# Performance work log

Hardware: AMD Instinct MI355X
Metric: run time of the kernel (lower is better)

## Reference

```python
import jax, jax.numpy as jnp
import numpy as np

N_NODES = 122880  # 4096 graphs * 30 nodes
N_EDGES = 983040


def gcn_conv(x, W, b, src, dst, n):
    """PyG GCNConv: symmetric-normalized aggregation with self-loops."""
    h = x @ W  # [n, out]
    loop = jnp.arange(n, dtype=src.dtype)
    s = jnp.concatenate([src, loop])
    d = jnp.concatenate([dst, loop])
    deg = jnp.zeros((n,), dtype=h.dtype).at[d].add(1.0)  # >=1 due to self loops
    dinv = jax.lax.rsqrt(deg)
    norm = dinv[s] * dinv[d]  # [E+n]
    out = jax.ops.segment_sum(h[s] * norm[:, None], d, num_segments=n)
    return out + b


def setup_inputs() -> dict:
    key = jax.random.key(0)
    ks = jax.random.split(key, 8)
    x = jax.random.normal(ks[0], (N_NODES, 64), dtype=jnp.float32)
    edge_index = jax.random.randint(ks[1], (2, N_EDGES), 0, N_NODES, dtype=jnp.int64)
    W1 = jax.random.normal(ks[2], (64, 128), dtype=jnp.float32) * (1.0 / np.sqrt(64))
    b1 = jnp.zeros((128,), dtype=jnp.float32)
    W2 = jax.random.normal(ks[3], (128, 64), dtype=jnp.float32) * (1.0 / np.sqrt(128))
    b2 = jnp.zeros((64,), dtype=jnp.float32)
    Wfc = jax.random.normal(ks[4], (1920, 1728), dtype=jnp.float32) * (1.0 / np.sqrt(1920))
    bfc = jnp.zeros((1728,), dtype=jnp.float32)
    return {"x": x, "edge_index": edge_index, "W1": W1, "b1": b1,
            "W2": W2, "b2": b2, "Wfc": Wfc, "bfc": bfc}


def reference(x, edge_index, W1, b1, W2, b2, Wfc, bfc):
    n = x.shape[0]
    src, dst = edge_index[0], edge_index[1]
    h = gcn_conv(x, W1, b1, src, dst, n)
    h = jax.nn.relu(h)  # dropout is identity in eval mode
    h = gcn_conv(h, W2, b2, src, dst, n)
    h = jax.nn.relu(h)
    h = h.reshape(-1, 64 * 30)  # [B, 1920], 30 nodes per graph
    return h @ Wfc + bfc  # [B, 1728]
```

## Files before the change

kernel.cpp:

```cpp
#include <hip/hip_runtime.h>
#include <hip/hip_bf16.h>

#define N_NODES 122880
#define N_EDGES 983040
#define NBKT 480
#define BCAP 2560
#define EPB 4096

typedef __hip_bfloat16 bf16;
typedef __attribute__((ext_vector_type(8))) short short8;
typedef __attribute__((ext_vector_type(4))) float floatx4;

__device__ __forceinline__ void gl_lds16(const void* g, void* l) {
    __builtin_amdgcn_global_load_lds(
        (const __attribute__((address_space(1))) void*)g,
        (__attribute__((address_space(3))) void*)l, 16, 0, 0);
}

__device__ __forceinline__ float bflo(unsigned u) {
    return __uint_as_float(u << 16);
}
__device__ __forceinline__ float bfhi(unsigned u) {
    return __uint_as_float(u & 0xffff0000u);
}

__global__ __launch_bounds__(256) void k_psort(const int* __restrict__ ei,
                                               int* __restrict__ gcur,
                                               unsigned* __restrict__ gbuf) {
    __shared__ int cur[NBKT];
    __shared__ int gb[NBKT];
    const int t = threadIdx.x;
    for (int i = t; i < NBKT; i += 256) cur[i] = 0;
    __syncthreads();
    const int base = blockIdx.x * EPB;
    unsigned pay[16];
    short bk[16], pib[16];
#pragma unroll
    for (int j = 0; j < 16; ++j) {
        int e = base + j * 256 + t;
        int d = ei[N_EDGES + e];
        int s = ei[e];
        bk[j] = (short)(d >> 8);
        pay[j] = (unsigned)(d & 255) | ((unsigned)s << 8);
        pib[j] = (short)atomicAdd(&cur[d >> 8], 1);
    }
    __syncthreads();
    for (int i = t; i < NBKT; i += 256) {
        int c = cur[i];
        gb[i] = c ? atomicAdd(&gcur[i * 16], c) : 0;
    }
    __syncthreads();
#pragma unroll
    for (int j = 0; j < 16; ++j) {
        int pos = gb[bk[j]] + pib[j];
        if (pos < BCAP) gbuf[bk[j] * BCAP + pos] = pay[j];
    }
}

__global__ __launch_bounds__(256) void k_bcsr(const int* __restrict__ gcur,
                                              const unsigned* __restrict__ gbuf,
                                              int* __restrict__ adj,
                                              unsigned* __restrict__ co,
                                              float* __restrict__ dinv) {
    __shared__ int hist[256];
    __shared__ int arr[256];
    __shared__ int exc[256];
    const int b = blockIdx.x, t = threadIdx.x;
    hist[t] = 0;
    __syncthreads();
    int E = gcur[b * 16];
    if (E > BCAP) E = BCAP;
    int dl[10], sv[10];
    short pb[10];
    int n = 0;
    for (int idx = t; idx < E; idx += 256) {
        unsigned p = gbuf[b * BCAP + idx];
        dl[n] = p & 255;
        sv[n] = (int)(p >> 8);
        pb[n] = (short)atomicAdd(&hist[dl[n]], 1);
        ++n;
    }
    __syncthreads();
    const int cnt_t = hist[t];
    arr[t] = cnt_t;
    __syncthreads();
    for (int d = 1; d < 256; d <<= 1) {
        int v = (t >= d) ? arr[t - d] : 0;
        __syncthreads();
        arr[t] += v;
        __syncthreads();
    }
    const int ex = arr[t] - cnt_t;
    exc[t] = ex;
    const int node = b * 256 + t;
    co[node] = ((unsigned)ex << 16) | (unsigned)cnt_t;
    dinv[node] = rsqrtf((float)cnt_t + 1.0f);
    __syncthreads();
    for (int j = 0; j < n; ++j)
        adj[b * BCAP + exc[dl[j]] + pb[j]] = sv[j];
}

__global__ __launch_bounds__(256) void k_xtobf(const float* __restrict__ x,
                                               bf16* __restrict__ xb) {
    int t = blockIdx.x * 256 + threadIdx.x;
    const float4 v = ((const float4*)x)[t];
    bf16* o = xb + t * 4;
    o[0] = __float2bfloat16(v.x);
    o[1] = __float2bfloat16(v.y);
    o[2] = __float2bfloat16(v.z);
    o[3] = __float2bfloat16(v.w);
}

__global__ __launch_bounds__(256) void k_convw(const float* __restrict__ W1,
                                               const float* __restrict__ W2,
                                               bf16* __restrict__ W1T,
                                               bf16* __restrict__ W2T) {
    int t = blockIdx.x * 256 + threadIdx.x;
    if (t < 64 * 128) {
        int k = t >> 7, n = t & 127;
        W1T[n * 64 + k] = __float2bfloat16(W1[t]);
    } else {
        int u = t - 64 * 128;
        int k = u >> 6, n = u & 63;
        W2T[n * 128 + k] = __float2bfloat16(W2[u]);
    }
}

__global__ __launch_bounds__(256) void k_transWfc(const float* __restrict__ W,
                                                  bf16* __restrict__ WT) {
    __shared__ float t[32][33];
    int tx = threadIdx.x, ty = threadIdx.y;
    int n0 = blockIdx.x * 32, k0 = blockIdx.y * 32;
#pragma unroll
    for (int j = 0; j < 4; ++j)
        t[ty + j * 8][tx] = W[(long)(k0 + ty + j * 8) * 1728 + n0 + tx];
    __syncthreads();
#pragma unroll
    for (int j = 0; j < 4; ++j)
        WT[(long)(n0 + ty + j * 8) * 1920 + k0 + tx] =
            __float2bfloat16(t[tx][ty + j * 8]);
}

template <bool BIAS_RELU>
__global__ __launch_bounds__(256) void k_agg(const bf16* __restrict__ xb,
                                             const float* __restrict__ dinv,
                                             const unsigned* __restrict__ co,
                                             const int* __restrict__ adj,
                                             const float* __restrict__ bias,
                                             bf16* __restrict__ out) {
    const int wave = threadIdx.x >> 6, lane = threadIdx.x & 63;
    const int half = lane >> 5, l32 = lane & 31;
    const int node = blockIdx.x * 8 + wave * 2 + half;

    const float di = dinv[node];
    const unsigned c_ = co[node];
    int c = (int)(c_ & 0xffffu);
    if (c > 32) c = 32;
    const int* al = adj + (node >> 8) * BCAP + (c_ >> 16);
    int   sl = (l32 < c) ? al[l32]  : 0;
    float wl = (l32 < c) ? dinv[sl] : 0.0f;

    const unsigned us = *(const unsigned*)(xb + ((long)node << 6) + (l32 << 1));
    float acc0 = di * bflo(us);
    float acc1 = di * bfhi(us);

    for (int p0 = 0; p0 < c; p0 += 8) {
        unsigned uu[8];
        float w8[8];
#pragma unroll
        for (int j = 0; j < 8; ++j) {
            int p = p0 + j;
            bool ok = p < c;
            int s = ok ? __shfl(sl, p, 32) : 0;
            w8[j] = ok ? __shfl(wl, p, 32) : 0.0f;
            uu[j] = *(const unsigned*)(xb + ((long)s << 6) + (l32 << 1));
        }
#pragma unroll
        for (int j = 0; j < 8; ++j) {
            acc0 += w8[j] * bflo(uu[j]);
            acc1 += w8[j] * bfhi(uu[j]);
        }
    }

    float r0 = di * acc0, r1 = di * acc1;
    if (BIAS_RELU) {
        r0 = fmaxf(r0 + bias[l32 * 2], 0.0f);
        r1 = fmaxf(r1 + bias[l32 * 2 + 1], 0.0f);
    }
    bf16* o = out + ((long)node << 6) + (l32 << 1);
    o[0] = __float2bfloat16(r0);
    o[1] = __float2bfloat16(r1);
}

template <bool RELU, bool BIAS, typename OutT>
__global__ __launch_bounds__(256) void gemm_bt(const bf16* __restrict__ A,
                                               const bf16* __restrict__ BT,
                                               const float* __restrict__ bias,
                                               OutT* __restrict__ C,
                                               int M, int N, int K) {
    __shared__ __align__(16) bf16 As[128 * 32];
    __shared__ __align__(16) bf16 Bs[64 * 32];
    const int tid = threadIdx.x;
    const int wave = tid >> 6, lane = tid & 63;
    const int quad = lane >> 4, l16 = lane & 15;
    const int bm = blockIdx.x * 128, bn = blockIdx.y * 64;
    const int wm = (wave & 1) * 64, wn = (wave >> 1) * 32;

    floatx4 acc[4][2];
#pragma unroll
    for (int i = 0; i < 4; ++i)
#pragma unroll
        for (int j = 0; j < 2; ++j)
            acc[i][j] = (floatx4){0.f, 0.f, 0.f, 0.f};

    const int r4 = tid >> 2;
    const int ch = (((tid & 3) ^ ((tid >> 3) & 3)) * 8);
    const bf16* gA0 = A + (long)(bm + r4) * K + ch;
    const bf16* gA1 = A + (long)(bm + r4 + 64) * K + ch;
    const bf16* gB  = BT + (long)(bn + r4) * K + ch;
    bf16* lA0 = As + wave * 512;
    bf16* lA1 = As + 2048 + wave * 512;
    bf16* lB  = Bs + wave * 512;

    const int rsw = (l16 >> 1) & 3;

    for (int k0 = 0; k0 < K; k0 += 32) {
        gl_lds16(gA0 + k0, lA0);
        gl_lds16(gA1 + k0, lA1);
        gl_lds16(gB + k0, lB);
        __syncthreads();
        short8 af[4], bfr[2];
#pragma unroll
        for (int im = 0; im < 4; ++im)
            af[im] = *(const short8*)(As + (wm + im * 16 + l16) * 32 +
                                      (quad ^ rsw) * 8);
#pragma unroll
        for (int in = 0; in < 2; ++in)
            bfr[in] = *(const short8*)(Bs + (wn + in * 16 + l16) * 32 +
                                       (quad ^ rsw) * 8);
#pragma unroll
        for (int im = 0; im < 4; ++im)
#pragma unroll
            for (int in = 0; in < 2; ++in)
                acc[im][in] = __builtin_amdgcn_mfma_f32_16x16x32_bf16(
                    af[im], bfr[in], acc[im][in], 0, 0, 0);
        __syncthreads();
    }

#pragma unroll
    for (int in = 0; in < 2; ++in) {
        int gcol = bn + wn + in * 16 + l16;
        float bv = BIAS ? bias[gcol] : 0.0f;
#pragma unroll
        for (int im = 0; im < 4; ++im) {
            int mrow = bm + wm + im * 16 + quad * 4;
#pragma unroll
            for (int r = 0; r < 4; ++r) {
                float v = acc[im][in][r] + bv;
                if (RELU) v = fmaxf(v, 0.0f);
                if constexpr (sizeof(OutT) == 2)
                    C[(long)(mrow + r) * N + gcol] = __float2bfloat16(v);
                else
                    C[(long)(mrow + r) * N + gcol] = v;
            }
        }
    }
}

extern "C" void kernel_launch(void* const* d_in, const int* in_sizes, int n_in,
                              void* d_out, int out_size, void* d_ws, size_t ws_size,
                              hipStream_t stream) {
    const float* x   = (const float*)d_in[0];
    const int*   ei  = (const int*)d_in[1];
    const float* W1  = (const float*)d_in[2];
    const float* b1  = (const float*)d_in[3];
    const float* W2  = (const float*)d_in[4];
    const float* b2  = (const float*)d_in[5];
    const float* Wfc = (const float*)d_in[6];
    const float* bfc = (const float*)d_in[7];

    char* p = (char*)d_ws;
    int*      gcur = (int*)p;      p += (size_t)NBKT * 16 * 4;
    unsigned* gbuf = (unsigned*)p; p += (size_t)NBKT * BCAP * 4;
    int*      adj  = (int*)p;      p += (size_t)NBKT * BCAP * 4;
    unsigned* co   = (unsigned*)p; p += (size_t)N_NODES * 4;
    float*    dinv = (float*)p;    p += (size_t)N_NODES * 4;
    bf16*     xb   = (bf16*)p;     p += (size_t)N_NODES * 64 * 2;
    bf16*     xa   = (bf16*)p;     p += (size_t)N_NODES * 64 * 2;
    bf16*     h1   = (bf16*)p;     p += (size_t)N_NODES * 128 * 2;
    bf16*     W1T  = (bf16*)p;     p += 128 * 64 * 2;
    bf16*     W2T  = (bf16*)p;     p += 64 * 128 * 2;
    bf16*     WfcT = (bf16*)p;     p += (size_t)1728 * 1920 * 2;

    hipMemsetAsync(gcur, 0, (size_t)NBKT * 16 * 4, stream);
    k_psort<<<N_EDGES / EPB, 256, 0, stream>>>(ei, gcur, gbuf);
    k_bcsr<<<NBKT, 256, 0, stream>>>(gcur, gbuf, adj, co, dinv);
    k_xtobf<<<N_NODES * 64 / 4 / 256, 256, 0, stream>>>(x, xb);
    k_convw<<<64, 256, 0, stream>>>(W1, W2, W1T, W2T);
    k_transWfc<<<dim3(54, 60), dim3(32, 8), 0, stream>>>(Wfc, WfcT);

    k_agg<false><<<N_NODES / 8, 256, 0, stream>>>(xb, dinv, co, adj, nullptr, xa);
    gemm_bt<true, true, bf16><<<dim3(960, 2), 256, 0, stream>>>(
        xa, W1T, b1, h1, N_NODES, 128, 64);
    bf16* g = xa;
    gemm_bt<false, false, bf16><<<dim3(960, 1), 256, 0, stream>>>(
        h1, W2T, nullptr, g, N_NODES, 64, 128);
    bf16* h2 = h1;
    k_agg<true><<<N_NODES / 8, 256, 0, stream>>>(g, dinv, co, adj, b2, h2);
    gemm_bt<false, true, float><<<dim3(32, 27), 256, 0, stream>>>(
        h2, WfcT, bfc, (float*)d_out, 4096, 1728, 1920);
}
```

Before: 264.2 us.

## Fuse the two GCN weight GEMMs into one kernel and register-prefetch gemm_bt

Adds a k_mlp kernel that computes relu(xa·W1+b1) for a 128-row tile, keeps the 128-wide intermediate in LDS, and multiplies it by W2 right away. This removes the global write and re-read of the N×128 h1 buffer and one kernel launch. The final FC gemm_bt also changes from direct global-to-LDS loads to loading the next K-slice into registers and then storing it to LDS, so the global load overlaps the MFMAs. The fused kernel uses more LDS (about 51 KB per block), which can lower occupancy.

```diff
diff --git a/kernel.cpp b/kernel.cpp
--- a/kernel.cpp
+++ b/kernel.cpp
@@ -190,6 +190,106 @@
     bf16* o = out + ((long)node << 6) + (l32 << 1);
     o[0] = __float2bfloat16(r0);
     o[1] = __float2bfloat16(r1);
+}
+
+__global__ __launch_bounds__(256) void k_mlp(const bf16* __restrict__ xa,
+                                             const bf16* __restrict__ W1T,
+                                             const bf16* __restrict__ W2T,
+                                             const float* __restrict__ b1,
+                                             bf16* __restrict__ g) {
+    __shared__ __align__(16) bf16 As[128 * 64];
+    __shared__ __align__(16) bf16 C1s[128 * 136];
+    const int tid = threadIdx.x;
+    const int wave = tid >> 6, lane = tid & 63;
+    const int quad = lane >> 4, l16 = lane & 15;
+    const int bm = blockIdx.x * 128;
+    const int wm = (wave & 1) * 64;
+    const int wn1 = (wave >> 1) * 64;
+    const int wn2 = (wave >> 1) * 32;
+
+#pragma unroll
+    for (int q = 0; q < 4; ++q) {
+        int G = q * 256 + tid;
+        int gc = (G & ~7) | ((G & 7) ^ ((G >> 3) & 7));
+        gl_lds16(xa + (long)bm * 64 + gc * 8, As + ((q * 4 + wave) * 64) * 8);
+    }
+    short8 w1f[2][4];
+#pragma unroll
+    for (int kc = 0; kc < 2; ++kc)
+#pragma unroll
+        for (int in = 0; in < 4; ++in)
+            w1f[kc][in] = *(const short8*)(W1T + (wn1 + in * 16 + l16) * 64 +
+                                           kc * 32 + quad * 8);
+    floatx4 acc1[4][4];
+#pragma unroll
+    for (int i = 0; i < 4; ++i)
+#pragma unroll
+        for (int j = 0; j < 4; ++j) acc1[i][j] = (floatx4){0.f, 0.f, 0.f, 0.f};
+    __syncthreads();
+
+#pragma unroll
+    for (int kc = 0; kc < 2; ++kc)
+#pragma unroll
+        for (int im = 0; im < 4; ++im) {
+            const int R = wm + im * 16 + l16;
+            short8 af = *(const short8*)(As + R * 64 +
+                                         (((kc * 4 + quad) ^ (R & 7)) * 8));
+#pragma unroll
+            for (int in = 0; in < 4; ++in)
+                acc1[im][in] = __builtin_amdgcn_mfma_f32_16x16x32_bf16(
+                    af, w1f[kc][in], acc1[im][in], 0, 0, 0);
+        }
+
+#pragma unroll
+    for (int in = 0; in < 4; ++in) {
+        const int col = wn1 + in * 16 + l16;
+        const float bv = b1[col];
+#pragma unroll
+        for (int im = 0; im < 4; ++im) {
+            const int row = wm + im * 16 + quad * 4;
+#pragma unroll
+            for (int r = 0; r < 4; ++r)
+                C1s[(row + r) * 136 + col] =
+                    __float2bfloat16(fmaxf(acc1[im][in][r] + bv, 0.0f));
+        }
+    }
+    short8 w2f[4][2];
+#pragma unroll
+    for (int kc = 0; kc < 4; ++kc)
+#pragma unroll
+        for (int in = 0; in < 2; ++in)
+            w2f[kc][in] = *(const short8*)(W2T + (wn2 + in * 16 + l16) * 128 +
+                                           kc * 32 + quad * 8);
+    floatx4 acc2[4][2];
+#pragma unroll
+    for (int i = 0; i < 4; ++i)
+#pragma unroll
+        for (int j = 0; j < 2; ++j) acc2[i][j] = (floatx4){0.f, 0.f, 0.f, 0.f};
+    __syncthreads();
+
+#pragma unroll
+    for (int kc = 0; kc < 4; ++kc)
+#pragma unroll
+        for (int im = 0; im < 4; ++im) {
+            short8 af = *(const short8*)(C1s + (wm + im * 16 + l16) * 136 +
+                                         kc * 32 + quad * 8);
+#pragma unroll
+            for (int in = 0; in < 2; ++in)
+                acc2[im][in] = __builtin_amdgcn_mfma_f32_16x16x32_bf16(
+                    af, w2f[kc][in], acc2[im][in], 0, 0, 0);
+        }
+
+#pragma unroll
+    for (int in = 0; in < 2; ++in) {
+        const int col = wn2 + in * 16 + l16;
+#pragma unroll
+        for (int im = 0; im < 4; ++im) {
+            const int row = bm + wm + im * 16 + quad * 4;
+#pragma unroll
+            for (int r = 0; r < 4; ++r)
+                g[(long)(row + r) * 64 + col] = __float2bfloat16(acc2[im][in][r]);
+        }
+    }
 }
 
 template <bool RELU, bool BIAS, typename OutT>
@@ -210,25 +310,32 @@
 #pragma unroll
     for (int i = 0; i < 4; ++i)
 #pragma unroll
-        for (int j = 0; j < 2; ++j)
-            acc[i][j] = (floatx4){0.f, 0.f, 0.f, 0.f};
+        for (int j = 0; j < 2; ++j) acc[i][j] = (floatx4){0.f, 0.f, 0.f, 0.f};
 
     const int r4 = tid >> 2;
-    const int ch = (((tid & 3) ^ ((tid >> 3) & 3)) * 8);
-    const bf16* gA0 = A + (long)(bm + r4) * K + ch;
-    const bf16* gA1 = A + (long)(bm + r4 + 64) * K + ch;
-    const bf16* gB  = BT + (long)(bn + r4) * K + ch;
-    bf16* lA0 = As + wave * 512;
-    bf16* lA1 = As + 2048 + wave * 512;
-    bf16* lB  = Bs + wave * 512;
+    const int cc = tid & 3;
+    const int slot = r4 * 32 + ((cc ^ ((r4 >> 1) & 3)) * 8);
+
+    const bf16* gA0 = A + (long)(bm + r4) * K + cc * 8;
+    const bf16* gA1 = A + (long)(bm + r4 + 64) * K + cc * 8;
+    const bf16* gB  = BT + (long)(bn + r4) * K + cc * 8;
+
+    uint4 ra0 = *(const uint4*)gA0;
+    uint4 ra1 = *(const uint4*)gA1;
+    uint4 rb  = *(const uint4*)gB;
 
     const int rsw = (l16 >> 1) & 3;
 
     for (int k0 = 0; k0 < K; k0 += 32) {
-        gl_lds16(gA0 + k0, lA0);
-        gl_lds16(gA1 + k0, lA1);
-        gl_lds16(gB + k0, lB);
+        *(uint4*)(As + slot) = ra0;
+        *(uint4*)(As + 2048 + slot) = ra1;
+        *(uint4*)(Bs + slot) = rb;
         __syncthreads();
+        if (k0 + 32 < K) {
+            ra0 = *(const uint4*)(gA0 + k0 + 32);
+            ra1 = *(const uint4*)(gA1 + k0 + 32);
+            rb  = *(const uint4*)(gB + k0 + 32);
+        }
         short8 af[4], bfr[2];
 #pragma unroll
         for (int im = 0; im < 4; ++im)
@@ -287,7 +394,8 @@
     float*    dinv = (float*)p;    p += (size_t)N_NODES * 4;
     bf16*     xb   = (bf16*)p;     p += (size_t)N_NODES * 64 * 2;
     bf16*     xa   = (bf16*)p;     p += (size_t)N_NODES * 64 * 2;
-    bf16*     h1   = (bf16*)p;     p += (size_t)N_NODES * 128 * 2;
+    bf16*     g    = (bf16*)p;     p += (size_t)N_NODES * 64 * 2;
+    bf16*     h2   = (bf16*)p;     p += (size_t)N_NODES * 64 * 2;
     bf16*     W1T  = (bf16*)p;     p += 128 * 64 * 2;
     bf16*     W2T  = (bf16*)p;     p += 64 * 128 * 2;
     bf16*     WfcT = (bf16*)p;     p += (size_t)1728 * 1920 * 2;
@@ -300,12 +408,7 @@
     k_transWfc<<<dim3(54, 60), dim3(32, 8), 0, stream>>>(Wfc, WfcT);
 
     k_agg<false><<<N_NODES / 8, 256, 0, stream>>>(xb, dinv, co, adj, nullptr, xa);
-    gemm_bt<true, true, bf16><<<dim3(960, 2), 256, 0, stream>>>(
-        xa, W1T, b1, h1, N_NODES, 128, 64);
-    bf16* g = xa;
-    gemm_bt<false, false, bf16><<<dim3(960, 1), 256, 0, stream>>>(
-        h1, W2T, nullptr, g, N_NODES, 64, 128);
-    bf16* h2 = h1;
+    k_mlp<<<N_NODES / 128, 256, 0, stream>>>(xa, W1T, W2T, b1, g);
     k_agg<true><<<N_NODES / 8, 256, 0, stream>>>(g, dinv, co, adj, b2, h2);
     gemm_bt<false, true, float><<<dim3(32, 27), 256, 0, stream>>>(
         h2, WfcT, bfc, (float*)d_out, 4096, 1728, 1920);
```

Result: faster. 255.1 us (-3.4%).
